# Performance work log

Measured on AMD Instinct MI355X. Metric: run time of the kernel, lower is better.

The kernel has to match this reference:

```python
import jax, jax.numpy as jnp
import numpy as np

B, L, DIN = 2048, 70, 15
HID, NF, K = 16, 4, 40          # hidden_units//2, n_features, kernel_size
C = DIN + 1 + NF                # 20 signature input channels (original + time + conv features)
Z0 = 64
SIG_CH = C + C * C + C ** 3     # 8420, depth-3 signature channels


def setup_inputs() -> dict:
    key = jax.random.key(0)
    ks = jax.random.split(key, 8)
    return {
        "observed_data": jax.random.normal(ks[0], (B, L, DIN), jnp.float32),
        "observed_tp": jnp.linspace(0.0, 1.0, L, dtype=jnp.float32),
        "conv1_w": jax.random.normal(ks[1], (HID, DIN, K), jnp.float32) / np.float32(np.sqrt(DIN * K)),
        "conv1_b": jnp.zeros((HID,), jnp.float32),
        "conv2_w": jax.random.normal(ks[2], (HID, HID), jnp.float32) / np.float32(np.sqrt(HID)),
        "conv2_b": jnp.zeros((HID,), jnp.float32),
        "conv3_w": jax.random.normal(ks[3], (NF, HID), jnp.float32) / np.float32(np.sqrt(HID)),
        "conv3_b": jnp.zeros((NF,), jnp.float32),
        "w_out": jax.random.normal(ks[4], (2 * Z0, SIG_CH), jnp.float32) * np.float32(np.sqrt(2.0 / (SIG_CH + 2 * Z0))),
        "b_out": jnp.zeros((2 * Z0,), jnp.float32),
    }


def _augment(x, w1, b1, w2, b2, w3, b3):
    # x: (B, L, DIN).  signatory.Augment: conv(K) -> relu -> conv1x1 -> relu -> conv1x1,
    # then concat [truncated original, time channel, conv features] along channels.
    xc = jnp.transpose(x, (0, 2, 1))                                   # (B, DIN, L)
    h = jax.lax.conv_general_dilated(xc, w1, (1,), 'VALID')            # (B, HID, Lp)
    h = h + b1[None, :, None]
    h = jnp.einsum('oc,bcl->bol', w2, jax.nn.relu(h)) + b2[None, :, None]
    h = jnp.einsum('oc,bcl->bol', w3, jax.nn.relu(h)) + b3[None, :, None]
    conv_out = jnp.transpose(h, (0, 2, 1))                             # (B, Lp, NF)
    Lp = conv_out.shape[1]
    orig = x[:, K - 1:, :]                                             # (B, Lp, DIN)
    t = jnp.linspace(0.0, 1.0, Lp, dtype=x.dtype)
    time = jnp.broadcast_to(t[None, :, None], (x.shape[0], Lp, 1))
    return jnp.concatenate([orig, time, conv_out], axis=2)             # (B, Lp, C)


def _signature_depth3(path):
    # Truncated (depth 3) path signature with basepoint=True, via Chen's identity:
    # S <- S \otimes exp(dx) over increments, zero basepoint prepended.
    incs = jnp.diff(path, axis=1, prepend=jnp.zeros_like(path[:, :1]))  # (B, Lp, C)
    incs = jnp.transpose(incs, (1, 0, 2))                               # (Lp, B, C)
    Bn, Cn = path.shape[0], path.shape[2]
    s1 = jnp.zeros((Bn, Cn), path.dtype)
    s2 = jnp.zeros((Bn, Cn, Cn), path.dtype)
    s3 = jnp.zeros((Bn, Cn, Cn, Cn), path.dtype)

    def step(carry, d):
        s1, s2, s3 = carry
        e2 = 0.5 * d[:, :, None] * d[:, None, :]                        # d\otimes d / 2
        e3 = (e2[:, :, :, None] * d[:, None, None, :]) / 3.0            # d^{\otimes 3} / 6
        n3 = (s3
              + s2[:, :, :, None] * d[:, None, None, :]
              + s1[:, :, None, None] * e2[:, None, :, :]
              + e3)
        n2 = s2 + s1[:, :, None] * d[:, None, :] + e2
        n1 = s1 + d
        return (n1, n2, n3), None

    (s1, s2, s3), _ = jax.lax.scan(step, (s1, s2, s3), incs)
    return jnp.concatenate([s1, s2.reshape(Bn, -1), s3.reshape(Bn, -1)], axis=1)


def reference(observed_data, observed_tp, conv1_w, conv1_b, conv2_w, conv2_b,
              conv3_w, conv3_b, w_out, b_out):
    # encode_obs_time=False -> observed_tp unused
    path = _augment(observed_data, conv1_w, conv1_b, conv2_w, conv2_b, conv3_w, conv3_b)
    sig = _signature_depth3(path)                                       # (B, SIG_CH)
    z = sig @ w_out.T + b_out                                           # (B, 2*Z0)
    mean_z0 = z[:, :Z0][None]                                           # (1, B, Z0)
    std_z0 = jax.nn.softplus(z[:, Z0:][None])                           # (1, B, Z0)
    return mean_z0, std_z0
```

## Files before the change

### kernel.cpp

```cpp
#include <hip/hip_runtime.h>
#include <math.h>

#define B_TOT 2048
#define D_INC 15
#define KW    40
#define CCH   20
#define LP    31
#define SIGCH 8420
#define SIGP  8448
#define NOUT  128
#define KSPLIT 11
#define KLEN  768

typedef _Float16 f16;
typedef _Float16 f16x8 __attribute__((ext_vector_type(8)));
typedef _Float16 f16x4 __attribute__((ext_vector_type(4)));
typedef _Float16 f16x2 __attribute__((ext_vector_type(2)));
typedef float    f32x4 __attribute__((ext_vector_type(4)));

__global__ __launch_bounds__(256) void k_prep(const float* __restrict__ w1,
                                              f16* __restrict__ wA)
{
    const int ln = threadIdx.x & 63;
    const int wv = threadIdx.x >> 6;
    const int h  = ln & 15;
    const int q4 = ln >> 4;
    for (int gi = 0; gi < 5; ++gi) {
        int g = wv * 5 + gi;
        f16x8 v;
#pragma unroll
        for (int j = 0; j < 8; ++j) {
            int kq = q4 * 8 + j;
            int kk = 2 * g + (kq >> 4);
            int c  = kq & 15;
            v[j] = (c < D_INC) ? (f16)w1[h * 600 + c * 40 + kk] : (f16)0.f;
        }
        *(f16x8*)(wA + g * 512 + ln * 8) = v;
    }
}

__global__ __launch_bounds__(256, 3) void k_augsig(
    const float* __restrict__ x,  const f16* __restrict__ wA, const float* __restrict__ b1,
    const float* __restrict__ w2, const float* __restrict__ b2,
    const float* __restrict__ w3, const float* __restrict__ b3,
    const float* __restrict__ w_out, f16* __restrict__ wh, f16* __restrict__ sig)
{
    if (blockIdx.x >= 512) {
        int t0 = (blockIdx.x - 512) * 256 + threadIdx.x;
        for (int chunk = t0; chunk < 128 * 1056; chunk += 8192) {
            int o  = chunk / 1056;
            int cw = chunk - o * 1056;
            int c0 = cw * 8;
            f16x8 v;
            if (c0 + 8 <= SIGCH) {
                const float* src = w_out + (size_t)o * SIGCH + c0;
                float4 a = *(const float4*)src;
                float4 b = *(const float4*)(src + 4);
                v = (f16x8){(f16)a.x,(f16)a.y,(f16)a.z,(f16)a.w,
                            (f16)b.x,(f16)b.y,(f16)b.z,(f16)b.w};
            } else {
#pragma unroll
                for (int e = 0; e < 8; ++e) {
                    int c = c0 + e;
                    v[e] = (c < SIGCH) ? (f16)w_out[(size_t)o * SIGCH + c] : (f16)0.f;
                }
            }
            *(f16x8*)(wh + (size_t)o * SIGP + c0) = v;
        }
        return;
    }

    __shared__ float pool[12388];
    float* xs    = pool;
    f16*   xp16  = (f16*)(pool + 4272);
    float* h1s   = (float*)xp16;
    float* pprev = pool + 9408;
    float* wsmall= pool + 12032;
    float* w2s = wsmall;        float* b2s = wsmall + 256;
    float* w3s = wsmall + 272;  float* b3s = wsmall + 336;
    float* b1s = wsmall + 340;

    const int tid  = threadIdx.x;
    const int b0   = blockIdx.x * 4;
    const int lane = tid & 63;
    const int w    = tid >> 6;
    const int n16  = lane & 15;
    const int q4   = lane >> 4;

    for (int i = tid; i < 4 * 1050; i += 256) {
        int bl = i / 1050; int t = i - bl * 1050;
        xs[bl * 1068 + t] = x[(size_t)b0 * 1050 + i];
    }
    if (tid < 256) w2s[tid] = w2[tid];
    if (tid < 16)  b2s[tid] = b2[tid];
    if (tid < 64)  w3s[tid] = w3[tid];
    if (tid < 4)   b3s[tid] = b3[tid];
    if (tid < 16)  b1s[tid] = b1[tid];

    f16x8 wa[20];
#pragma unroll
    for (int g = 0; g < 20; ++g) wa[g] = *(const f16x8*)(wA + g * 512 + lane * 8);
    __syncthreads();

    for (int r = tid; r < 280; r += 256) {
        int bl = r / 70; int pos = r - bl * 70;
        const float* src = xs + bl * 1068 + pos * 15;
        f16* dst = xp16 + bl * 1152 + pos * 16;
#pragma unroll
        for (int c = 0; c < 15; ++c) dst[c] = (f16)src[c];
        dst[15] = (f16)0.f;
    }
    __syncthreads();

    f32x4 cacc[2];
#pragma unroll
    for (int tile = 0; tile < 2; ++tile) {
        const int pos0 = tile * 15;
        f32x4 acc = {0.f, 0.f, 0.f, 0.f};
#pragma unroll
        for (int g = 0; g < 20; ++g) {
            const f16x8 bf = *(const f16x8*)&xp16[w * 1152 +
                (pos0 + n16 + 2 * g + (q4 >> 1)) * 16 + (q4 & 1) * 8];
            acc = __builtin_amdgcn_mfma_f32_16x16x32_f16(wa[g], bf, acc, 0, 0, 0);
        }
        cacc[tile] = acc;
    }
    __syncthreads();

#pragma unroll
    for (int tile = 0; tile < 2; ++tile) {
        int pos = tile * 15 + n16;
#pragma unroll
        for (int r = 0; r < 4; ++r) {
            int h = q4 * 4 + r;
            h1s[(w * 31 + pos) * 17 + h] = fmaxf(cacc[tile][r] + b1s[h], 0.f);
        }
    }
    __syncthreads();

    if (tid < 124) {
        const int bl2 = tid / 31;
        const int pos = tid - bl2 * 31;
        float hr[16];
#pragma unroll
        for (int c2 = 0; c2 < 16; ++c2) hr[c2] = h1s[tid * 17 + c2];
        float h2[16];
#pragma unroll
        for (int o = 0; o < 16; ++o) {
            float s = b2s[o];
#pragma unroll
            for (int c2 = 0; c2 < 16; ++c2) s += w2s[o * 16 + c2] * hr[c2];
            h2[o] = fmaxf(s, 0.f);
        }
        float h3[4];
#pragma unroll
        for (int f = 0; f < 4; ++f) {
            float s = b3s[f];
#pragma unroll
            for (int c2 = 0; c2 < 16; ++c2) s += w3s[f * 16 + c2] * h2[c2];
            h3[f] = s;
        }
        float* pr = pprev + bl2 * 656 + 20 + pos * 20;
#pragma unroll
        for (int d = 0; d < D_INC; ++d) pr[d] = xs[bl2 * 1068 + (pos + 39) * 15 + d];
        pr[15] = (float)pos * (1.0f / 30.0f);
#pragma unroll
        for (int f = 0; f < 4; ++f) pr[16 + f] = h3[f];
    } else {
        int z = tid - 124;
        if (z < 80) pprev[(z / 20) * 656 + (z % 20)] = 0.f;
    }
    __syncthreads();

    float* pp   = pprev + w * 656;
    f16*   scr  = (f16*)pool + w * 4704;
    f16*   dtr  = scr;
    f16*   atr  = scr + 800;
    f16*   etr  = scr + 1600;
    f16*   Vb   = scr + 2400;

    for (int e = lane; e < 620; e += 64) {
        int c = e / 31, t = e - c * 31;
        float p0 = pp[t * 20 + c];
        float d  = pp[(t + 1) * 20 + c] - p0;
        dtr[c * 40 + t] = (f16)d;
        atr[c * 40 + t] = (f16)(p0 + 0.5f * d);
        etr[c * 40 + t] = (f16)(0.5f * p0 + d * (1.0f / 6.0f));
    }
    if (lane < 20) {
        dtr[lane * 40 + 31] = (f16)0.f;
        atr[lane * 40 + 31] = (f16)0.f;
        etr[lane * 40 + 31] = (f16)0.f;
    }
    __syncthreads();

    if (lane < 20) {
        f16* vr = Vb + lane * 72;
        float s = 0.f;
        for (int t = 30; t >= 0; --t) {
            float dv = (float)dtr[lane * 40 + t];
            vr[t]      = (f16)s;
            vr[32 + t] = (f16)dv;
            s += dv;
        }
        vr[31] = (f16)0.f;
        vr[63] = (f16)0.f;
    } else if (lane == 20) {
        f16* vr = Vb + 20 * 72;
        for (int k = 0; k < 64; ++k) vr[k] = (k < 31) ? (f16)1.f : (f16)0.f;
    }
    for (int e = lane; e < 11 * 32; e += 64) {
        int row = 21 + (e >> 5);
        int kk  = (e & 31) * 2;
        *(f16x2*)(Vb + row * 72 + kk) = (f16x2){(f16)0.f, (f16)0.f};
    }
    __syncthreads();

    f16x8 bf[2][2];
#pragma unroll
    for (int kc = 0; kc < 2; ++kc)
#pragma unroll
        for (int nt = 0; nt < 2; ++nt)
            bf[kc][nt] = *(const f16x8*)(Vb + (nt * 16 + n16) * 72 + kc * 32 + q4 * 8);

    const int b = b0 + w;
    f16* sg = sig + (size_t)b * SIGP;

    for (int mt = 0; mt < 25; ++mt) {
        const int p = mt * 16 + n16;
        const int i = p / 20, j = p - i * 20;
        f16x8 av = *(const f16x8*)(atr + i * 40 + q4 * 8);
        f16x8 ev = *(const f16x8*)(etr + i * 40 + q4 * 8);
        f16x8 dv = *(const f16x8*)(dtr + j * 40 + q4 * 8);
        f16x8 uf = av * dv;
        f16x8 ef = ev * dv;

        f32x4 a0 = {0.f,0.f,0.f,0.f}, a1 = {0.f,0.f,0.f,0.f};
        a0 = __builtin_amdgcn_mfma_f32_16x16x32_f16(bf[0][0], uf, a0, 0, 0, 0);
        a0 = __builtin_amdgcn_mfma_f32_16x16x32_f16(bf[1][0], ef, a0, 0, 0, 0);
        a1 = __builtin_amdgcn_mfma_f32_16x16x32_f16(bf[0][1], uf, a1, 0, 0, 0);
        a1 = __builtin_amdgcn_mfma_f32_16x16x32_f16(bf[1][1], ef, a1, 0, 0, 0);

        f16x4 s0 = {(f16)a0[0], (f16)a0[1], (f16)a0[2], (f16)a0[3]};
        *(f16x4*)(sg + 420 + p * 20 + q4 * 4) = s0;
        if (q4 == 0) {
            f16x4 s1v = {(f16)a1[0], (f16)a1[1], (f16)a1[2], (f16)a1[3]};
            *(f16x4*)(sg + 420 + p * 20 + 16) = s1v;
        } else if (q4 == 1) {
            sg[20 + p] = (f16)a1[0];
        }
    }

    if (lane < 20) sg[lane] = (f16)pp[620 + lane];
    if (lane < 28) sg[SIGCH + lane] = (f16)0.f;
}

__global__ __launch_bounds__(256) void k_gemm(const f16* __restrict__ sigh,
                                              const f16* __restrict__ wh,
                                              float* __restrict__ z_part)
{
    __shared__ f16 As[2048];
    __shared__ f16 Bs[8192];
    const int tid = threadIdx.x;
    const int l   = tid & 63;
    const int wv  = tid >> 6;
    const int mt  = blockIdx.x / KSPLIT;
    const int s   = blockIdx.x - mt * KSPLIT;
    const int m0  = mt * 32;
    const int kb  = s * KLEN;

    const f32x4 z4 = {0.f, 0.f, 0.f, 0.f};
    f32x4 acc[2][2];
    acc[0][0] = z4; acc[0][1] = z4; acc[1][0] = z4; acc[1][1] = z4;

    const size_t gA = (size_t)(m0 + (tid & 31)) * SIGP + kb + (tid >> 5) * 8;
    size_t gB[4];
#pragma unroll
    for (int r = 0; r < 4; ++r) {
        int slot = r * 256 + tid;
        gB[r] = (size_t)(slot & 127) * SIGP + kb + (slot >> 7) * 8;
    }

    f16x8 aR = *(const f16x8*)(sigh + gA);
    f16x8 bR[4];
#pragma unroll
    for (int r = 0; r < 4; ++r) bR[r] = *(const f16x8*)(wh + gB[r]);

    const int kg   = l >> 4;
    const int mrow = l & 15;

    for (int ch = 0; ch < 12; ++ch) {
        *(f16x8*)&As[tid * 8] = aR;
#pragma unroll
        for (int r = 0; r < 4; ++r) *(f16x8*)&Bs[(r * 256 + tid) * 8] = bR[r];
        __syncthreads();

        if (ch < 11) {
            int koff = (ch + 1) * 64;
            aR = *(const f16x8*)(sigh + gA + koff);
#pragma unroll
            for (int r = 0; r < 4; ++r) bR[r] = *(const f16x8*)(wh + gB[r] + koff);
        }

#pragma unroll
        for (int kc = 0; kc < 2; ++kc) {
            f16x8 aF[2], bF[2];
#pragma unroll
            for (int m2 = 0; m2 < 2; ++m2)
                aF[m2] = *(const f16x8*)&As[((kc * 4 + kg) * 32 + m2 * 16 + mrow) * 8];
#pragma unroll
            for (int n2 = 0; n2 < 2; ++n2)
                bF[n2] = *(const f16x8*)&Bs[((kc * 4 + kg) * 128 + wv * 32 + n2 * 16 + mrow) * 8];
#pragma unroll
            for (int m2 = 0; m2 < 2; ++m2)
#pragma unroll
                for (int n2 = 0; n2 < 2; ++n2)
                    acc[m2][n2] = __builtin_amdgcn_mfma_f32_16x16x32_f16(aF[m2], bF[n2], acc[m2][n2], 0, 0, 0);
        }
        __syncthreads();
    }

#pragma unroll
    for (int m2 = 0; m2 < 2; ++m2) {
#pragma unroll
        for (int n2 = 0; n2 < 2; ++n2) {
            int n = wv * 32 + n2 * 16 + (l & 15);
#pragma unroll
            for (int r = 0; r < 4; ++r) {
                int m = m0 + m2 * 16 + (l >> 4) * 4 + r;
                z_part[((size_t)s * B_TOT + m) * NOUT + n] = acc[m2][n2][r];
            }
        }
    }
}

__global__ __launch_bounds__(256) void k_final(const float* __restrict__ z_part,
                                               const float* __restrict__ b_out,
                                               float* __restrict__ out)
{
    int idx = blockIdx.x * 256 + threadIdx.x;
    int b = idx >> 7;
    int o = idx & 127;
    float z = b_out[o];
#pragma unroll
    for (int s = 0; s < KSPLIT; ++s) z += z_part[((size_t)s * B_TOT + b) * NOUT + o];
    if (o < 64) {
        out[(size_t)b * 64 + o] = z;
    } else {
        float sp = fmaxf(z, 0.f) + log1pf(expf(-fabsf(z)));
        out[131072 + (size_t)b * 64 + (o - 64)] = sp;
    }
}

extern "C" void kernel_launch(void* const* d_in, const int* in_sizes, int n_in,
                              void* d_out, int out_size, void* d_ws, size_t ws_size,
                              hipStream_t stream)
{
    const float* x     = (const float*)d_in[0];
    const float* w1    = (const float*)d_in[2];
    const float* b1    = (const float*)d_in[3];
    const float* w2    = (const float*)d_in[4];
    const float* b2    = (const float*)d_in[5];
    const float* w3    = (const float*)d_in[6];
    const float* b3    = (const float*)d_in[7];
    const float* w_out = (const float*)d_in[8];
    const float* b_out = (const float*)d_in[9];
    float* out = (float*)d_out;

    float* ws    = (float*)d_ws;
    f16*   sigh  = (f16*)ws;
    f16*   wh    = (f16*)(ws + 8650752);
    f16*   wA    = (f16*)(ws + 9191424);
    float* zpart = ws + 9196544;

    hipLaunchKernelGGL(k_prep,   dim3(1),    dim3(256), 0, stream, w1, wA);
    hipLaunchKernelGGL(k_augsig, dim3(544),  dim3(256), 0, stream,
                       x, wA, b1, w2, b2, w3, b3, w_out, wh, sigh);
    hipLaunchKernelGGL(k_gemm,   dim3(704),  dim3(256), 0, stream, sigh, wh, zpart);
    hipLaunchKernelGGL(k_final,  dim3(1024), dim3(256), 0, stream, zpart, b_out, out);
}
```

Before: 134.9 us.

## Load GEMM fragments directly from global, move weight cast to prep, vectorize final

The split-K GEMM no longer stages tiles through shared memory with barriers. Each wave now reads its MFMA fragments straight from global memory, and the kernel gets a 4-blocks-per-CU launch bound. The w_out fp16 conversion moves from extra blocks of the augment/signature kernel into the prep kernel, and the final reduction now uses float4 loads and stores. This removes LDS traffic and synchronisation, at the cost of redundant global/L2 reads across waves and less coalesced 16-byte strided accesses.

```diff
diff --git a/kernel.cpp b/kernel.cpp
--- a/kernel.cpp
+++ b/kernel.cpp
@@ -19,23 +19,49 @@
 typedef float    f32x4 __attribute__((ext_vector_type(4)));
 
 __global__ __launch_bounds__(256) void k_prep(const float* __restrict__ w1,
-                                              f16* __restrict__ wA)
-{
-    const int ln = threadIdx.x & 63;
-    const int wv = threadIdx.x >> 6;
-    const int h  = ln & 15;
-    const int q4 = ln >> 4;
-    for (int gi = 0; gi < 5; ++gi) {
-        int g = wv * 5 + gi;
+                                              const float* __restrict__ w_out,
+                                              f16* __restrict__ wA,
+                                              f16* __restrict__ wh)
+{
+    if (blockIdx.x == 0) {
+        const int ln = threadIdx.x & 63;
+        const int wv = threadIdx.x >> 6;
+        const int h  = ln & 15;
+        const int q4 = ln >> 4;
+        for (int gi = 0; gi < 5; ++gi) {
+            int g = wv * 5 + gi;
+            f16x8 v;
+#pragma unroll
+            for (int j = 0; j < 8; ++j) {
+                int kq = q4 * 8 + j;
+                int kk = 2 * g + (kq >> 4);
+                int c  = kq & 15;
+                v[j] = (c < D_INC) ? (f16)w1[h * 600 + c * 40 + kk] : (f16)0.f;
+            }
+            *(f16x8*)(wA + g * 512 + ln * 8) = v;
+        }
+        return;
+    }
+    int t0 = (blockIdx.x - 1) * 256 + threadIdx.x;
+    for (int chunk = t0; chunk < 128 * 1056; chunk += 8192) {
+        int o  = chunk / 1056;
+        int cw = chunk - o * 1056;
+        int c0 = cw * 8;
         f16x8 v;
-#pragma unroll
-        for (int j = 0; j < 8; ++j) {
-            int kq = q4 * 8 + j;
-            int kk = 2 * g + (kq >> 4);
-            int c  = kq & 15;
-            v[j] = (c < D_INC) ? (f16)w1[h * 600 + c * 40 + kk] : (f16)0.f;
-        }
-        *(f16x8*)(wA + g * 512 + ln * 8) = v;
+        if (c0 + 8 <= SIGCH) {
+            const float* src = w_out + (size_t)o * SIGCH + c0;
+            float4 a = *(const float4*)src;
+            float4 b = *(const float4*)(src + 4);
+            v = (f16x8){(f16)a.x,(f16)a.y,(f16)a.z,(f16)a.w,
+                        (f16)b.x,(f16)b.y,(f16)b.z,(f16)b.w};
+        } else {
+#pragma unroll
+            for (int e = 0; e < 8; ++e) {
+                int c = c0 + e;
+                v[e] = (c < SIGCH) ? (f16)w_out[(size_t)o * SIGCH + c] : (f16)0.f;
+            }
+        }
+        *(f16x8*)(wh + (size_t)o * SIGP + c0) = v;
     }
 }
 
@@ -43,33 +69,8 @@
     const float* __restrict__ x,  const f16* __restrict__ wA, const float* __restrict__ b1,
     const float* __restrict__ w2, const float* __restrict__ b2,
     const float* __restrict__ w3, const float* __restrict__ b3,
-    const float* __restrict__ w_out, f16* __restrict__ wh, f16* __restrict__ sig)
-{
-    if (blockIdx.x >= 512) {
-        int t0 = (blockIdx.x - 512) * 256 + threadIdx.x;
-        for (int chunk = t0; chunk < 128 * 1056; chunk += 8192) {
-            int o  = chunk / 1056;
-            int cw = chunk - o * 1056;
-            int c0 = cw * 8;
-            f16x8 v;
-            if (c0 + 8 <= SIGCH) {
-                const float* src = w_out + (size_t)o * SIGCH + c0;
-                float4 a = *(const float4*)src;
-                float4 b = *(const float4*)(src + 4);
-                v = (f16x8){(f16)a.x,(f16)a.y,(f16)a.z,(f16)a.w,
-                            (f16)b.x,(f16)b.y,(f16)b.z,(f16)b.w};
-            } else {
-#pragma unroll
-                for (int e = 0; e < 8; ++e) {
-                    int c = c0 + e;
-                    v[e] = (c < SIGCH) ? (f16)w_out[(size_t)o * SIGCH + c] : (f16)0.f;
-                }
-            }
-            *(f16x8*)(wh + (size_t)o * SIGP + c0) = v;
-        }
-        return;
-    }
-
+    f16* __restrict__ sig)
+{
     __shared__ float pool[12388];
     float* xs    = pool;
     f16*   xp16  = (f16*)(pool + 4272);
@@ -255,12 +256,10 @@
     if (lane < 28) sg[SIGCH + lane] = (f16)0.f;
 }
 
-__global__ __launch_bounds__(256) void k_gemm(const f16* __restrict__ sigh,
-                                              const f16* __restrict__ wh,
-                                              float* __restrict__ z_part)
-{
-    __shared__ f16 As[2048];
-    __shared__ f16 Bs[8192];
+__global__ __launch_bounds__(256, 4) void k_gemm(const f16* __restrict__ sigh,
+                                                 const f16* __restrict__ wh,
+                                                 float* __restrict__ z_part)
+{
     const int tid = threadIdx.x;
     const int l   = tid & 63;
     const int wv  = tid >> 6;
@@ -268,56 +267,29 @@
     const int s   = blockIdx.x - mt * KSPLIT;
     const int m0  = mt * 32;
     const int kb  = s * KLEN;
+    const int kg   = l >> 4;
+    const int mrow = l & 15;
+
+    const f16* a0p = sigh + (size_t)(m0 + mrow) * SIGP + kb + kg * 8;
+    const f16* a1p = a0p + (size_t)16 * SIGP;
+    const f16* b0p = wh   + (size_t)(wv * 32 + mrow) * SIGP + kb + kg * 8;
+    const f16* b1p = b0p + (size_t)16 * SIGP;
 
     const f32x4 z4 = {0.f, 0.f, 0.f, 0.f};
     f32x4 acc[2][2];
     acc[0][0] = z4; acc[0][1] = z4; acc[1][0] = z4; acc[1][1] = z4;
 
-    const size_t gA = (size_t)(m0 + (tid & 31)) * SIGP + kb + (tid >> 5) * 8;
-    size_t gB[4];
-#pragma unroll
-    for (int r = 0; r < 4; ++r) {
-        int slot = r * 256 + tid;
-        gB[r] = (size_t)(slot & 127) * SIGP + kb + (slot >> 7) * 8;
-    }
-
-    f16x8 aR = *(const f16x8*)(sigh + gA);
-    f16x8 bR[4];
-#pragma unroll
-    for (int r = 0; r < 4; ++r) bR[r] = *(const f16x8*)(wh + gB[r]);
-
-    const int kg   = l >> 4;
-    const int mrow = l & 15;
-
-    for (int ch = 0; ch < 12; ++ch) {
-        *(f16x8*)&As[tid * 8] = aR;
-#pragma unroll
-        for (int r = 0; r < 4; ++r) *(f16x8*)&Bs[(r * 256 + tid) * 8] = bR[r];
-        __syncthreads();
-
-        if (ch < 11) {
-            int koff = (ch + 1) * 64;
-            aR = *(const f16x8*)(sigh + gA + koff);
-#pragma unroll
-            for (int r = 0; r < 4; ++r) bR[r] = *(const f16x8*)(wh + gB[r] + koff);
-        }
-
-#pragma unroll
-        for (int kc = 0; kc < 2; ++kc) {
-            f16x8 aF[2], bF[2];
-#pragma unroll
-            for (int m2 = 0; m2 < 2; ++m2)
-                aF[m2] = *(const f16x8*)&As[((kc * 4 + kg) * 32 + m2 * 16 + mrow) * 8];
-#pragma unroll
-            for (int n2 = 0; n2 < 2; ++n2)
-                bF[n2] = *(const f16x8*)&Bs[((kc * 4 + kg) * 128 + wv * 32 + n2 * 16 + mrow) * 8];
-#pragma unroll
-            for (int m2 = 0; m2 < 2; ++m2)
-#pragma unroll
-                for (int n2 = 0; n2 < 2; ++n2)
-                    acc[m2][n2] = __builtin_amdgcn_mfma_f32_16x16x32_f16(aF[m2], bF[n2], acc[m2][n2], 0, 0, 0);
-        }
-        __syncthreads();
+#pragma unroll 2
+    for (int ks = 0; ks < 24; ++ks) {
+        const int ko = ks * 32;
+        f16x8 aF0 = *(const f16x8*)(a0p + ko);
+        f16x8 aF1 = *(const f16x8*)(a1p + ko);
+        f16x8 bF0 = *(const f16x8*)(b0p + ko);
+        f16x8 bF1 = *(const f16x8*)(b1p + ko);
+        acc[0][0] = __builtin_amdgcn_mfma_f32_16x16x32_f16(aF0, bF0, acc[0][0], 0, 0, 0);
+        acc[0][1] = __builtin_amdgcn_mfma_f32_16x16x32_f16(aF0, bF1, acc[0][1], 0, 0, 0);
+        acc[1][0] = __builtin_amdgcn_mfma_f32_16x16x32_f16(aF1, bF0, acc[1][0], 0, 0, 0);
+        acc[1][1] = __builtin_amdgcn_mfma_f32_16x16x32_f16(aF1, bF1, acc[1][1], 0, 0, 0);
     }
 
 #pragma unroll
@@ -339,16 +311,23 @@
                                                float* __restrict__ out)
 {
     int idx = blockIdx.x * 256 + threadIdx.x;
-    int b = idx >> 7;
-    int o = idx & 127;
-    float z = b_out[o];
-#pragma unroll
-    for (int s = 0; s < KSPLIT; ++s) z += z_part[((size_t)s * B_TOT + b) * NOUT + o];
-    if (o < 64) {
-        out[(size_t)b * 64 + o] = z;
+    int b  = idx >> 5;
+    int o4 = (idx & 31) << 2;
+    float4 z = *(const float4*)(b_out + o4);
+#pragma unroll
+    for (int s = 0; s < KSPLIT; ++s) {
+        const float4 p = *(const float4*)(z_part + ((size_t)s * B_TOT + b) * NOUT + o4);
+        z.x += p.x; z.y += p.y; z.z += p.z; z.w += p.w;
+    }
+    if (o4 < 64) {
+        *(float4*)(out + (size_t)b * 64 + o4) = z;
     } else {
-        float sp = fmaxf(z, 0.f) + log1pf(expf(-fabsf(z)));
-        out[131072 + (size_t)b * 64 + (o - 64)] = sp;
+        float4 sp;
+        sp.x = fmaxf(z.x, 0.f) + log1pf(expf(-fabsf(z.x)));
+        sp.y = fmaxf(z.y, 0.f) + log1pf(expf(-fabsf(z.y)));
+        sp.z = fmaxf(z.z, 0.f) + log1pf(expf(-fabsf(z.z)));
+        sp.w = fmaxf(z.w, 0.f) + log1pf(expf(-fabsf(z.w)));
+        *(float4*)(out + 131072 + (size_t)b * 64 + (o4 - 64)) = sp;
     }
 }
 
@@ -373,9 +352,9 @@
     f16*   wA    = (f16*)(ws + 9191424);
     float* zpart = ws + 9196544;
 
-    hipLaunchKernelGGL(k_prep,   dim3(1),    dim3(256), 0, stream, w1, wA);
-    hipLaunchKernelGGL(k_augsig, dim3(544),  dim3(256), 0, stream,
-                       x, wA, b1, w2, b2, w3, b3, w_out, wh, sigh);
+    hipLaunchKernelGGL(k_prep,   dim3(33),   dim3(256), 0, stream, w1, w_out, wA, wh);
+    hipLaunchKernelGGL(k_augsig, dim3(512),  dim3(256), 0, stream,
+                       x, wA, b1, w2, b2, w3, b3, sigh);
     hipLaunchKernelGGL(k_gemm,   dim3(704),  dim3(256), 0, stream, sigh, wh, zpart);
-    hipLaunchKernelGGL(k_final,  dim3(1024), dim3(256), 0, stream, zpart, b_out, out);
-}
+    hipLaunchKernelGGL(k_final,  dim3(256),  dim3(256), 0, stream, zpart, b_out, out);
+}
```

After: 144.8 us. +7.4%, slower.
